# Kernel tuning notes

Measured on AMD Instinct MI355X. Metric: run time of the kernel, lower is better.

The kernel has to match this reference:

```python
import jax, jax.numpy as jnp
import numpy as np

B, Q, K, D = 16, 2048, 2048, 128
NEG = -1000000.0  # matches torch module's mask fill value (not -inf)


def setup_inputs() -> dict:
    key = jax.random.key(0)
    kq, kk, kv, kl = jax.random.split(key, 4)
    q = jax.random.normal(kq, (B, Q, D), dtype=jnp.float32)
    k = jax.random.normal(kk, (B, K, D), dtype=jnp.float32)
    v = jax.random.normal(kv, (B, K, D), dtype=jnp.float32)
    valid_lens = jax.random.randint(kl, (B, 1), 0, K, dtype=jnp.int32)
    return {"q": q, "k": k, "v": v, "valid_lens": valid_lens}


def reference(q, k, v, valid_lens):
    d = q.shape[-1]
    # scores: (B, Q, K)
    weight = jnp.einsum('bqd,bkd->bqk', q, k) / jnp.sqrt(jnp.asarray(d, q.dtype))
    # mask: key position j valid iff j < valid_len[b]; broadcast over query dim
    mask = jnp.arange(k.shape[1])[None, None, :] < valid_lens[:, :, None]  # (B,1,K)
    weight = jnp.where(mask, weight, NEG)
    score = jax.nn.softmax(weight, axis=-1)
    return jnp.einsum('bqk,bkv->bqv', score, v)
```

## Files before the change

### kernel.cpp

```cpp
#include <hip/hip_runtime.h>

constexpr int NB = 16;
constexpr int NQ = 2048;
constexpr int NK = 2048;
constexpr int ND = 128;
constexpr int KVBLK = 64;
constexpr int NTILE = NK / KVBLK;
constexpr int TILE_USH = KVBLK * ND;
constexpr float SCALE2 = 0.12751744751442557f;

typedef __attribute__((ext_vector_type(4))) float f4;
typedef __attribute__((ext_vector_type(16))) float f32x16;
typedef __attribute__((ext_vector_type(8))) unsigned short us8;
typedef __attribute__((ext_vector_type(8))) __bf16 bf16x8;
typedef __attribute__((ext_vector_type(4))) unsigned int u32x4;

static __device__ __forceinline__ unsigned short f2bf(float f) {
    unsigned u = __builtin_bit_cast(unsigned, f);
    u += 0x7fffu + ((u >> 16) & 1u);
    return (unsigned short)(u >> 16);
}
static __device__ __forceinline__ f4 splat4(float x) { f4 r = {x,x,x,x}; return r; }

static __device__ __forceinline__ float fexp2(float x) {
    float r;
    asm("v_exp_f32 %0, %1" : "=v"(r) : "v"(x));
    return r;
}

static __device__ __forceinline__ void load_lds16(const unsigned short* g, unsigned short* l) {
    __builtin_amdgcn_global_load_lds(
        (const __attribute__((address_space(1))) void*)g,
        (__attribute__((address_space(3))) void*)l,
        16, 0, 0);
}

static __device__ __forceinline__ unsigned cvt_pk_bf16(float lo, float hi) {
    unsigned r;
    asm("v_cvt_pk_bf16_f32 %0, %1, %2" : "=v"(r) : "v"(lo), "v"(hi));
    return r;
}

__global__ __launch_bounds__(256)
void prep_kv5(const float* __restrict__ kg, const float* __restrict__ vg,
              const int* __restrict__ vlen,
              unsigned short* __restrict__ wk, unsigned short* __restrict__ wvt)
{
    const int b   = blockIdx.y;
    const int t   = blockIdx.x;
    const int kv0 = t * KVBLK;

    {
        const int v = vlen[b];
        const int Leff = (v <= 0) ? NK : v;
        if (kv0 >= Leff) return;
    }

    const int t0  = threadIdx.x;

    __shared__ __align__(16) unsigned short vl[64 * 136];

    {
        const int kv = t0 >> 2;
        const int c  = t0 & 3;
        const float* gp = kg + (size_t)(b * NK + kv0 + kv) * ND + c * 32;
        unsigned short* ob = wk + (size_t)(b * NTILE + t) * TILE_USH;
        #pragma unroll
        for (int g = 0; g < 4; ++g) {
            f4 f0 = *(const f4*)(gp + g * 8);
            f4 f1 = *(const f4*)(gp + g * 8 + 4);
            us8 w;
            #pragma unroll
            for (int i = 0; i < 4; ++i) { w[i] = f2bf(f0[i]); w[i+4] = f2bf(f1[i]); }
            const int d0 = c * 32 + g * 8;
            const int f  = (kv >> 5) * 8 + (d0 >> 4);
            const int off = f * 512 + ((d0 >> 3) & 1) * 256 + (kv & 31) * 8;
            *(us8*)(ob + off) = w;
        }
    }
    {
        const int kv = t0 >> 2;
        const int d0 = (t0 & 3) * 32;
        const float* gp = vg + (size_t)(b * NK + kv0 + kv) * ND + d0;
        unsigned short* lb = &vl[kv * 136 + d0];
        #pragma unroll
        for (int g = 0; g < 4; ++g) {
            f4 f0 = *(const f4*)(gp + g * 8);
            f4 f1 = *(const f4*)(gp + g * 8 + 4);
            us8 w;
            #pragma unroll
            for (int i = 0; i < 4; ++i) { w[i] = f2bf(f0[i]); w[i+4] = f2bf(f1[i]); }
            *(us8*)(lb + g * 8) = w;
        }
    }
    __syncthreads();
    {
        unsigned short* ob = wvt + (size_t)(b * NTILE + t) * TILE_USH;
        #pragma unroll
        for (int iter = 0; iter < 4; ++iter) {
            const int cid = iter * 256 + t0;
            const int f   = cid >> 6;
            const int l   = cid & 63;
            const int kb  = (f >> 2) * 16 + (l >> 5) * 8;
            const int d   = (f & 3) * 32 + (l & 31);
            us8 w;
            #pragma unroll
            for (int j = 0; j < 8; ++j) w[j] = vl[(kb + j) * 136 + d];
            *(us8*)(ob + cid * 8) = w;
        }
    }
}

__global__ __launch_bounds__(256, 2)
void attn_fused17(const float* __restrict__ qg, const int* __restrict__ vlen,
                  const unsigned short* __restrict__ wk,
                  const unsigned short* __restrict__ wvt,
                  float* __restrict__ og)
{
    const int bid  = blockIdx.x;
    const int half = bid >> 8;
    const int j    = bid & 255;
    const int rank = half ? (15 - (j & 7)) : (j & 7);
    const int qc   = j >> 3;
    const int q0   = qc * 64;

    int b = 0;
    {
        int Ls[16];
        #pragma unroll
        for (int i = 0; i < 16; ++i) {
            const int v = vlen[i];
            Ls[i] = (v <= 0) ? NK : v;
        }
        #pragma unroll
        for (int bb = 0; bb < 16; ++bb) {
            int r = 0;
            #pragma unroll
            for (int cc = 0; cc < 16; ++cc)
                r += (Ls[cc] > Ls[bb] || (Ls[cc] == Ls[bb] && cc < bb)) ? 1 : 0;
            if (r == rank) b = bb;
        }
    }

    const int tid  = threadIdx.x;
    const int wid  = tid >> 6;
    const int grp  = wid >> 1;
    const int qw   = wid & 1;
    const int lane = tid & 63;
    const int lq   = lane & 31;
    const int hi   = lane >> 5;

    const int L = vlen[b];
    const bool uniform = (L <= 0);
    const int Leff = uniform ? NK : L;
    const int ntiles = (Leff + KVBLK - 1) / KVBLK;
    const int ng    = (ntiles + 1 - grp) >> 1;
    const int niter = (ntiles + 1) >> 1;

    __shared__ __align__(16) unsigned short smem[2][2 * TILE_USH];

    bf16x8 aq[8];
    {
        const float* qp = qg + (size_t)(b * NQ + q0 + qw * 32 + lq) * ND + hi * 8;
        #pragma unroll
        for (int c = 0; c < 8; ++c) {
            f4 f0 = *(const f4*)(qp + c * 16);
            f4 f1 = *(const f4*)(qp + c * 16 + 4);
            us8 u;
            #pragma unroll
            for (int i = 0; i < 4; ++i) {
                u[i]     = f2bf(f0[i] * SCALE2);
                u[i + 4] = f2bf(f1[i] * SCALE2);
            }
            aq[c] = __builtin_bit_cast(bf16x8, u);
        }
    }

    const unsigned short* kbg = wk  + (size_t)b * NTILE * TILE_USH;
    const unsigned short* vbg = wvt + (size_t)b * NTILE * TILE_USH;

    const unsigned short* sbase = qw ? vbg : kbg;
    unsigned short* sdst = &smem[grp][qw * 8192];
    const int s_off = lane * 8;

    float m_r = -__builtin_inff();
    float l_r = 0.f;
    f32x16 accO[4];
    #pragma unroll
    for (int dc = 0; dc < 4; ++dc)
        #pragma unroll
        for (int r = 0; r < 16; ++r) accO[dc][r] = 0.f;

    if (grp < ntiles) {
        const unsigned short* src = sbase + (size_t)grp * TILE_USH + s_off;
        #pragma unroll
        for (int jj = 0; jj < 16; ++jj) load_lds16(src + jj * 512, sdst + jj * 512);
    }
    __syncthreads();

    for (int i = 0; i < niter; ++i) {
        const int tile = 2 * i + grp;
        const unsigned short* kl  = &smem[grp][0];
        const unsigned short* vl2 = &smem[grp][8192];
        const bool act = (i < ng);

        us8 kf[16], vf[16];
        f32x16 sA, sB;
        if (act) {
            #pragma unroll
            for (int c = 0; c < 16; ++c)
                kf[c] = *(const us8*)&kl[c * 512 + lane * 8];
            #pragma unroll
            for (int r = 0; r < 16; ++r) { sA[r] = 0.f; sB[r] = 0.f; }
            #pragma unroll
            for (int c = 0; c < 8; ++c) {
                sA = __builtin_amdgcn_mfma_f32_32x32x16_bf16(
                    __builtin_bit_cast(bf16x8, kf[c]), aq[c], sA, 0, 0, 0);
                sB = __builtin_amdgcn_mfma_f32_32x32x16_bf16(
                    __builtin_bit_cast(bf16x8, kf[8 + c]), aq[c], sB, 0, 0, 0);
            }
            __builtin_amdgcn_sched_barrier(0);
            #pragma unroll
            for (int f = 0; f < 16; ++f)
                vf[f] = *(const us8*)&vl2[f * 512 + lane * 8];
        }

        __syncthreads();

        {
            const int tn = tile + 2;
            if (tn < ntiles) {
                const unsigned short* src = sbase + (size_t)tn * TILE_USH + s_off;
                #pragma unroll
                for (int jj = 0; jj < 16; ++jj) load_lds16(src + jj * 512, sdst + jj * 512);
            }
        }

        if (act) {
            const int kv0 = tile * KVBLK;

            if (uniform) {
                #pragma unroll
                for (int r = 0; r < 16; ++r) { sA[r] = 0.f; sB[r] = 0.f; }
            } else {
                const int lim0 = L - kv0 - 4 * hi;
                const int lim1 = lim0 - 32;
                #pragma unroll
                for (int r = 0; r < 16; ++r) {
                    const int rc = (r & 3) + 8 * (r >> 2);
                    sA[r] = (rc >= lim0) ? -__builtin_inff() : sA[r];
                    sB[r] = (rc >= lim1) ? -__builtin_inff() : sB[r];
                }
            }

            float tt[11];
            #pragma unroll
            for (int g3 = 0; g3 < 5; ++g3)
                tt[g3] = fmaxf(fmaxf(sA[3 * g3], sA[3 * g3 + 1]), sA[3 * g3 + 2]);
            tt[5] = fmaxf(fmaxf(sA[15], sB[0]), sB[1]);
            #pragma unroll
            for (int g3 = 0; g3 < 4; ++g3)
                tt[6 + g3] = fmaxf(fmaxf(sB[3 * g3 + 2], sB[3 * g3 + 3]), sB[3 * g3 + 4]);
            tt[10] = fmaxf(sB[14], sB[15]);
            const float u0 = fmaxf(fmaxf(tt[0], tt[1]), tt[2]);
            const float u1 = fmaxf(fmaxf(tt[3], tt[4]), tt[5]);
            const float u2 = fmaxf(fmaxf(tt[6], tt[7]), tt[8]);
            const float u3 = fmaxf(tt[9], tt[10]);
            const float pm = fmaxf(fmaxf(u0, u1), fmaxf(u2, u3));
            float pmax = fmaxf(pm, __shfl_xor(pm, 32));

            if (__any(pmax > m_r)) {
                const float mnew = fmaxf(m_r, pmax);
                const float sc = fexp2(m_r - mnew);
                m_r = mnew;
                l_r *= sc;
                #pragma unroll
                for (int r = 0; r < 16; ++r) {
                    const int src = ((r & 3) + 8 * (r >> 2) + 4 * hi) + (lane & 32);
                    const float scr = __shfl(sc, src);
                    accO[0][r] *= scr; accO[1][r] *= scr;
                    accO[2][r] *= scr; accO[3][r] *= scr;
                }
            }

            float p0[16], p1[16];
            #pragma unroll
            for (int r = 0; r < 16; ++r) {
                p0[r] = fexp2(sA[r] - m_r);
                p1[r] = fexp2(sB[r] - m_r);
            }
            float sm[8];
            #pragma unroll
            for (int i2 = 0; i2 < 8; ++i2)
                sm[i2] = (p0[i2] + p0[i2 + 8]) + (p1[i2] + p1[i2 + 8]);
            #pragma unroll
            for (int i2 = 0; i2 < 4; ++i2) sm[i2] += sm[i2 + 4];
            float rsum = (sm[0] + sm[1]) + (sm[2] + sm[3]);
            rsum += __shfl_xor(rsum, 32);
            l_r += rsum;

            unsigned cw[16];
            #pragma unroll
            for (int i2 = 0; i2 < 8; ++i2) cw[i2] = cvt_pk_bf16(p0[2 * i2], p0[2 * i2 + 1]);
            #pragma unroll
            for (int i2 = 0; i2 < 8; ++i2) cw[8 + i2] = cvt_pk_bf16(p1[2 * i2], p1[2 * i2 + 1]);

            bf16x8 pa[4];
            #pragma unroll
            for (int ks = 0; ks < 4; ++ks) {
                const int a = 4 * ks;
                const unsigned u = hi ? cw[a]     : cw[a + 2];
                const unsigned v = hi ? cw[a + 1] : cw[a + 3];
                const unsigned up = __shfl_xor((int)u, 32);
                const unsigned vp = __shfl_xor((int)v, 32);
                u32x4 w;
                w[0] = hi ? up        : cw[a];
                w[1] = hi ? vp        : cw[a + 1];
                w[2] = hi ? cw[a + 2] : up;
                w[3] = hi ? cw[a + 3] : vp;
                pa[ks] = __builtin_bit_cast(bf16x8, w);
            }

            #pragma unroll
            for (int dc = 0; dc < 4; ++dc) {
                #pragma unroll
                for (int ks = 0; ks < 4; ++ks) {
                    accO[dc] = __builtin_amdgcn_mfma_f32_32x32x16_bf16(
                        pa[ks], __builtin_bit_cast(bf16x8, vf[ks * 4 + dc]), accO[dc], 0, 0, 0);
                }
            }
        }

        __syncthreads();
    }

    float* accb = (float*)&smem[0][0];
    float* mlb  = accb + 8192;
    if (grp == 1) {
        #pragma unroll
        for (int dc = 0; dc < 4; ++dc) {
            #pragma unroll
            for (int q4 = 0; q4 < 4; ++q4) {
                f4 v;
                #pragma unroll
                for (int c = 0; c < 4; ++c) v[c] = accO[dc][q4 * 4 + c];
                *(f4*)&accb[(((qw * 16 + dc * 4 + q4) * 64) + lane) * 4] = v;
            }
        }
        if (hi == 0) {
            mlb[qw * 32 + lq]      = m_r;
            mlb[64 + qw * 32 + lq] = l_r;
        }
    }
    __syncthreads();
    if (grp == 0) {
        const float m1 = mlb[qw * 32 + lq];
        const float l1 = mlb[64 + qw * 32 + lq];
        const float m  = fmaxf(m_r, m1);
        const float a0 = fexp2(m_r - m), a1 = fexp2(m1 - m);
        const float linv = 1.0f / (a0 * l_r + a1 * l1);
        const float s0v = a0 * linv, s1v = a1 * linv;
        float* ob = og + (size_t)(b * NQ + q0 + qw * 32) * ND;
        #pragma unroll
        for (int dc = 0; dc < 4; ++dc) {
            #pragma unroll
            for (int q4 = 0; q4 < 4; ++q4) {
                f4 o1 = *(const f4*)&accb[(((qw * 16 + dc * 4 + q4) * 64) + lane) * 4];
                #pragma unroll
                for (int c = 0; c < 4; ++c) {
                    const int r = q4 * 4 + c;
                    const int row = c + 8 * q4 + 4 * hi;
                    const float s0r = __shfl(s0v, row + (lane & 32));
                    const float s1r = __shfl(s1v, row + (lane & 32));
                    ob[(size_t)row * ND + dc * 32 + lq] = accO[dc][r] * s0r + o1[c] * s1r;
                }
            }
        }
    }
}

__global__ __launch_bounds__(256, 2)
void attn_fused(const float* __restrict__ qg, const float* __restrict__ kg,
                const float* __restrict__ vg, const int* __restrict__ vlen,
                float* __restrict__ og)
{
    const int b    = blockIdx.y;
    const int q0   = blockIdx.x * 64;
    const int tid  = threadIdx.x;
    const int wid  = tid >> 6;
    const int lane = tid & 63;
    const int lrow = lane & 15;
    const int lgrp = lane >> 4;
    constexpr float SCALE = 0.08838834764831844f;

    const int L = vlen[b];
    const bool uniform = (L <= 0);
    const int Leff = uniform ? NK : L;
    const int nt32 = (Leff + 31) / 32;

    __shared__ __align__(16) unsigned short kt[32 * 136];
    __shared__ __align__(16) unsigned short vt[128 * 40];
    __shared__ __align__(16) float pt[4][16 * 36];

    bf16x8 aqf[4];
    {
        const float* qp = qg + (size_t)(b * NQ + q0 + wid * 16 + lrow) * ND + lgrp * 8;
        #pragma unroll
        for (int c = 0; c < 4; ++c) {
            f4 f0 = *(const f4*)(qp + c * 32);
            f4 f1 = *(const f4*)(qp + c * 32 + 4);
            us8 u;
            #pragma unroll
            for (int i = 0; i < 4; ++i) {
                u[i]     = f2bf(f0[i] * SCALE);
                u[i + 4] = f2bf(f1[i] * SCALE);
            }
            aqf[c] = __builtin_bit_cast(bf16x8, u);
        }
    }

    float m_r[4], l_r[4];
    f4 accO[8];
    #pragma unroll
    for (int r = 0; r < 4; ++r) { m_r[r] = -__builtin_inff(); l_r[r] = 0.f; }
    #pragma unroll
    for (int dc = 0; dc < 8; ++dc) accO[dc] = splat4(0.f);

    for (int t = 0; t < nt32; ++t) {
        const int kv0 = t * 32;
        __syncthreads();
        {
            const int r  = tid >> 3;
            const int c0 = (tid & 7) * 16;
            const float* gp = kg + (size_t)(b * NK + kv0 + r) * ND + c0;
            f4 f0 = *(const f4*)(gp);
            f4 f1 = *(const f4*)(gp + 4);
            f4 f2 = *(const f4*)(gp + 8);
            f4 f3 = *(const f4*)(gp + 12);
            us8 w0, w1;
            #pragma unroll
            for (int i = 0; i < 4; ++i) {
                w0[i]     = f2bf(f0[i]);
                w0[i + 4] = f2bf(f1[i]);
                w1[i]     = f2bf(f2[i]);
                w1[i + 4] = f2bf(f3[i]);
            }
            unsigned short* dst = &kt[r * 136 + c0];
            *(us8*)(dst)     = w0;
            *(us8*)(dst + 8) = w1;
        }
        {
            const int d  = tid & 127;
            const int g2 = tid >> 7;
            const float* gp = vg + (size_t)(b * NK + kv0 + g2 * 16) * ND + d;
            us8 w0, w1;
            #pragma unroll
            for (int jj = 0; jj < 8; ++jj) {
                w0[jj] = f2bf(gp[(size_t)jj * ND]);
                w1[jj] = f2bf(gp[(size_t)(jj + 8) * ND]);
            }
            unsigned short* dst = &vt[d * 40 + g2 * 16];
            *(us8*)(dst)     = w0;
            *(us8*)(dst + 8) = w1;
        }
        __syncthreads();

        f4 s0 = splat4(0.f), s1 = splat4(0.f);
        #pragma unroll
        for (int c = 0; c < 4; ++c) {
            bf16x8 bk0 = __builtin_bit_cast(bf16x8,
                *(const us8*)&kt[lrow * 136 + c * 32 + lgrp * 8]);
            s0 = __builtin_amdgcn_mfma_f32_16x16x32_bf16(aqf[c], bk0, s0, 0, 0, 0);
            bf16x8 bk1 = __builtin_bit_cast(bf16x8,
                *(const us8*)&kt[(16 + lrow) * 136 + c * 32 + lgrp * 8]);
            s1 = __builtin_amdgcn_mfma_f32_16x16x32_bf16(aqf[c], bk1, s1, 0, 0, 0);
        }

        const int col0 = kv0 + lrow;
        if (uniform) {
            s0 = splat4(0.f);
            s1 = splat4(0.f);
        } else {
            if (col0 >= L)      s0 = splat4(-__builtin_inff());
            if (col0 + 16 >= L) s1 = splat4(-__builtin_inff());
        }

        float pm[4];
        #pragma unroll
        for (int r = 0; r < 4; ++r) pm[r] = fmaxf(s0[r], s1[r]);
        #pragma unroll
        for (int off = 8; off > 0; off >>= 1) {
            #pragma unroll
            for (int r = 0; r < 4; ++r)
                pm[r] = fmaxf(pm[r], __shfl_xor(pm[r], off));
        }
        float pr0[4], pr1[4], rs[4], sc[4];
        #pragma unroll
        for (int r = 0; r < 4; ++r) {
            float mn = fmaxf(m_r[r], pm[r]);
            sc[r]  = __expf(m_r[r] - mn);
            m_r[r] = mn;
            pr0[r] = __expf(s0[r] - mn);
            pr1[r] = __expf(s1[r] - mn);
            rs[r]  = pr0[r] + pr1[r];
        }
        #pragma unroll
        for (int off = 8; off > 0; off >>= 1) {
            #pragma unroll
            for (int r = 0; r < 4; ++r)
                rs[r] += __shfl_xor(rs[r], off);
        }
        #pragma unroll
        for (int r = 0; r < 4; ++r) l_r[r] = l_r[r] * sc[r] + rs[r];
        #pragma unroll
        for (int dc = 0; dc < 8; ++dc) {
            #pragma unroll
            for (int r = 0; r < 4; ++r) accO[dc][r] *= sc[r];
        }

        float* pw = pt[wid];
        #pragma unroll
        for (int r = 0; r < 4; ++r) {
            pw[(lgrp * 4 + r) * 36 + lrow]      = pr0[r];
            pw[(lgrp * 4 + r) * 36 + 16 + lrow] = pr1[r];
        }
        asm volatile("s_waitcnt lgkmcnt(0)" ::: "memory");
        f4 a0 = *(const f4*)&pw[lrow * 36 + lgrp * 8];
        f4 a1 = *(const f4*)&pw[lrow * 36 + lgrp * 8 + 4];
        us8 au;
        #pragma unroll
        for (int i = 0; i < 4; ++i) { au[i] = f2bf(a0[i]); au[i + 4] = f2bf(a1[i]); }
        bf16x8 ap = __builtin_bit_cast(bf16x8, au);

        #pragma unroll
        for (int dc = 0; dc < 8; ++dc) {
            bf16x8 bv = __builtin_bit_cast(bf16x8,
                *(const us8*)&vt[(dc * 16 + lrow) * 40 + lgrp * 8]);
            accO[dc] = __builtin_amdgcn_mfma_f32_16x16x32_bf16(ap, bv, accO[dc], 0, 0, 0);
        }
    }

    float inv[4];
    #pragma unroll
    for (int r = 0; r < 4; ++r) inv[r] = 1.0f / l_r[r];
    float* op = og + (size_t)(b * NQ + q0 + wid * 16) * ND;
    #pragma unroll
    for (int dc = 0; dc < 8; ++dc) {
        #pragma unroll
        for (int r = 0; r < 4; ++r)
            op[(lgrp * 4 + r) * ND + dc * 16 + lrow] = accO[dc][r] * inv[r];
    }
}

extern "C" void kernel_launch(void* const* d_in, const int* in_sizes, int n_in,
                              void* d_out, int out_size, void* d_ws, size_t ws_size,
                              hipStream_t stream) {
    (void)in_sizes; (void)n_in; (void)out_size;
    const float* q  = (const float*)d_in[0];
    const float* k  = (const float*)d_in[1];
    const float* v  = (const float*)d_in[2];
    const int*   vl = (const int*)d_in[3];
    float* out = (float*)d_out;

    const size_t kvbytes = 2 * (size_t)NB * NK * ND * sizeof(unsigned short);
    if (ws_size >= kvbytes) {
        unsigned short* wk  = (unsigned short*)d_ws;
        unsigned short* wvt = wk + (size_t)NB * NK * ND;
        hipLaunchKernelGGL(prep_kv5, dim3(NTILE, NB), dim3(256), 0, stream, k, v, vl, wk, wvt);
        hipLaunchKernelGGL(attn_fused17, dim3((NQ / 64) * NB), dim3(256), 0, stream,
                           q, vl, wk, wvt, out);
    } else {
        hipLaunchKernelGGL(attn_fused, dim3(NQ / 64, NB), dim3(256), 0, stream,
                           q, k, v, vl, out);
    }
}
```

Measured before the change: 56.79 us.

## Double-buffer K tiles in LDS and read V fragments directly from global

K tiles are now staged into a double-buffered LDS array, with the prefetch of the next tile issued at the top of each iteration. V fragments are loaded straight from global memory into registers instead of through LDS. This removes one of the two barriers per iteration and halves the LDS traffic per tile. In exchange, V reads become global loads whose latency may not be hidden before the PV MFMAs. The LDS footprint stays the same because the K buffers reuse the space V used to occupy.

Measured after the change: 55.01 us. 1.03x faster.

```diff
diff --git a/kernel.cpp b/kernel.cpp
--- a/kernel.cpp
+++ b/kernel.cpp
@@ -112,7 +112,7 @@
 }
 
 __global__ __launch_bounds__(256, 2)
-void attn_fused17(const float* __restrict__ qg, const int* __restrict__ vlen,
+void attn_fused18(const float* __restrict__ qg, const int* __restrict__ vlen,
                   const unsigned short* __restrict__ wk,
                   const unsigned short* __restrict__ wvt,
                   float* __restrict__ og)
@@ -157,7 +157,7 @@
     const int ng    = (ntiles + 1 - grp) >> 1;
     const int niter = (ntiles + 1) >> 1;
 
-    __shared__ __align__(16) unsigned short smem[2][2 * TILE_USH];
+    __shared__ __align__(16) unsigned short kbuf[2][2][8192];
 
     bf16x8 aq[8];
     {
@@ -179,9 +179,7 @@
     const unsigned short* kbg = wk  + (size_t)b * NTILE * TILE_USH;
     const unsigned short* vbg = wvt + (size_t)b * NTILE * TILE_USH;
 
-    const unsigned short* sbase = qw ? vbg : kbg;
-    unsigned short* sdst = &smem[grp][qw * 8192];
-    const int s_off = lane * 8;
+    const int s_off = qw * 4096 + lane * 8;
 
     float m_r = -__builtin_inff();
     float l_r = 0.f;
@@ -192,24 +190,36 @@
         for (int r = 0; r < 16; ++r) accO[dc][r] = 0.f;
 
     if (grp < ntiles) {
-        const unsigned short* src = sbase + (size_t)grp * TILE_USH + s_off;
-        #pragma unroll
-        for (int jj = 0; jj < 16; ++jj) load_lds16(src + jj * 512, sdst + jj * 512);
+        const unsigned short* src = kbg + (size_t)grp * TILE_USH + s_off;
+        unsigned short* dst = &kbuf[grp][0][qw * 4096];
+        #pragma unroll
+        for (int jj = 0; jj < 8; ++jj) load_lds16(src + jj * 512, dst + jj * 512);
     }
     __syncthreads();
 
     for (int i = 0; i < niter; ++i) {
         const int tile = 2 * i + grp;
-        const unsigned short* kl  = &smem[grp][0];
-        const unsigned short* vl2 = &smem[grp][8192];
-        const bool act = (i < ng);
-
-        us8 kf[16], vf[16];
-        f32x16 sA, sB;
-        if (act) {
+        const int buf  = i & 1;
+
+        {
+            const int tn = tile + 2;
+            if (tn < ntiles) {
+                const unsigned short* src = kbg + (size_t)tn * TILE_USH + s_off;
+                unsigned short* dst = &kbuf[grp][buf ^ 1][qw * 4096];
+                #pragma unroll
+                for (int jj = 0; jj < 8; ++jj) load_lds16(src + jj * 512, dst + jj * 512);
+            }
+        }
+
+        if (i < ng) {
+            const int kv0 = tile * KVBLK;
+            const unsigned short* kl = &kbuf[grp][buf][0];
+
+            us8 kf[16];
             #pragma unroll
             for (int c = 0; c < 16; ++c)
                 kf[c] = *(const us8*)&kl[c * 512 + lane * 8];
+            f32x16 sA, sB;
             #pragma unroll
             for (int r = 0; r < 16; ++r) { sA[r] = 0.f; sB[r] = 0.f; }
             #pragma unroll
@@ -220,24 +230,14 @@
                     __builtin_bit_cast(bf16x8, kf[8 + c]), aq[c], sB, 0, 0, 0);
             }
             __builtin_amdgcn_sched_barrier(0);
-            #pragma unroll
-            for (int f = 0; f < 16; ++f)
-                vf[f] = *(const us8*)&vl2[f * 512 + lane * 8];
-        }
-
-        __syncthreads();
-
-        {
-            const int tn = tile + 2;
-            if (tn < ntiles) {
-                const unsigned short* src = sbase + (size_t)tn * TILE_USH + s_off;
-                #pragma unroll
-                for (int jj = 0; jj < 16; ++jj) load_lds16(src + jj * 512, sdst + jj * 512);
-            }
-        }
-
-        if (act) {
-            const int kv0 = tile * KVBLK;
+
+            us8 vf[16];
+            {
+                const unsigned short* vsrc = vbg + (size_t)tile * TILE_USH + lane * 8;
+                #pragma unroll
+                for (int f = 0; f < 16; ++f)
+                    vf[f] = *(const us8*)(vsrc + f * 512);
+            }
 
             if (uniform) {
                 #pragma unroll
@@ -334,7 +334,7 @@
         __syncthreads();
     }
 
-    float* accb = (float*)&smem[0][0];
+    float* accb = (float*)&kbuf[0][0][0];
     float* mlb  = accb + 8192;
     if (grp == 1) {
         #pragma unroll
@@ -567,7 +567,7 @@
         unsigned short* wk  = (unsigned short*)d_ws;
         unsigned short* wvt = wk + (size_t)NB * NK * ND;
         hipLaunchKernelGGL(prep_kv5, dim3(NTILE, NB), dim3(256), 0, stream, k, v, vl, wk, wvt);
-        hipLaunchKernelGGL(attn_fused17, dim3((NQ / 64) * NB), dim3(256), 0, stream,
+        hipLaunchKernelGGL(attn_fused18, dim3((NQ / 64) * NB), dim3(256), 0, stream,
                            q, vl, wk, wvt, out);
     } else {
         hipLaunchKernelGGL(attn_fused, dim3(NQ / 64, NB), dim3(256), 0, stream,
```
